# Performance work log

Measured on AMD Instinct MI355X. Metric: run time of the kernel, lower is better.

The kernel has to match this reference:

```python
import jax, jax.numpy as jnp
import numpy as np

B, T, D, H, Dh = 2, 2048, 2048, 16, 128


def setup_inputs() -> dict:
    key = jax.random.key(0)
    ks = jax.random.split(key, 9)
    s = 0.02
    return {
        "x": jax.random.normal(ks[0], (B, T, D), jnp.float32),
        "Wq": jax.random.normal(ks[1], (H, D, Dh), jnp.float32) * s,
        "bq": jax.random.normal(ks[2], (H, Dh), jnp.float32) * s,
        "Wk": jax.random.normal(ks[3], (H, D, Dh), jnp.float32) * s,
        "bk": jax.random.normal(ks[4], (H, Dh), jnp.float32) * s,
        "Wv": jax.random.normal(ks[5], (H, D, Dh), jnp.float32) * s,
        "bv": jax.random.normal(ks[6], (H, Dh), jnp.float32) * s,
        "Wp": jax.random.normal(ks[7], (D, D), jnp.float32) * s,
        "bp": jax.random.normal(ks[8], (D,), jnp.float32) * s,
    }


def reference(x, Wq, bq, Wk, bk, Wv, bv, Wp, bp):
    # per-head projections (stacked): [B, H, T, Dh]
    q = jnp.einsum("btd,hde->bhte", x, Wq) + bq[None, :, None, :]
    k = jnp.einsum("btd,hde->bhte", x, Wk) + bk[None, :, None, :]
    v = jnp.einsum("btd,hde->bhte", x, Wv) + bv[None, :, None, :]
    scale = Dh ** -0.5
    att = jnp.einsum("bhte,bhse->bhts", q, k) * scale  # [B,H,T,T]
    causal = jnp.tril(jnp.ones((T, T), bool))
    att = jnp.where(causal, att, -jnp.inf)
    att = jax.nn.softmax(att, axis=-1)
    # dropout p=0.0 -> identity
    out = jnp.einsum("bhts,bhse->bhte", att, v)  # [B,H,T,Dh]
    out = out.transpose(0, 2, 1, 3).reshape(B, T, H * Dh)  # concat heads
    return out @ Wp.T if False else jnp.einsum("btd,ed->bte", out, Wp.T) if False else out @ Wp + bp
```

## Files before the change

### kernel.cpp

```cpp
#include <hip/hip_runtime.h>
#include <hip/hip_bf16.h>
#include <math.h>

typedef __attribute__((ext_vector_type(8))) short bf16x8;
typedef __attribute__((ext_vector_type(4))) float f32x4;
typedef __attribute__((ext_vector_type(16))) float f32x16;

__device__ __forceinline__ unsigned short f2b(float f) {
    union { float f; unsigned u; } a; a.f = f;
    unsigned r = a.u + 0x7FFFu + ((a.u >> 16) & 1u);
    return (unsigned short)(r >> 16);
}

__device__ __forceinline__ void gl_lds16(const unsigned short* g, unsigned short* l) {
    __builtin_amdgcn_global_load_lds(
        (const __attribute__((address_space(1))) unsigned int*)g,
        (__attribute__((address_space(3))) unsigned int*)l,
        16, 0, 0);
}

#define SCALE2 0.12751744716529944f

__global__ __launch_bounds__(256) void prep_kernel(
    const float* __restrict__ x,
    const float* __restrict__ Wq, const float* __restrict__ Wk,
    const float* __restrict__ Wv, const float* __restrict__ Wp,
    unsigned short* __restrict__ xb, unsigned short* __restrict__ wt,
    unsigned short* __restrict__ wpt) {
    __shared__ float tile_s[32][33];
    int bid = blockIdx.x;
    int tx = threadIdx.x, ty = threadIdx.y;
    if (bid < 12288) {
        int z = bid >> 8;
        int tile = bid & 255;
        int c0 = (tile & 3) * 32, r0 = (tile >> 2) * 32;
        int mat = z >> 4, hh = z & 15;
        const float* src = ((mat == 0) ? Wq : (mat == 1) ? Wk : Wv) + (size_t)hh * 2048 * 128;
        unsigned short* dst = wt + (size_t)z * 128 * 2048;
#pragma unroll
        for (int i = 0; i < 32; i += 8)
            tile_s[ty + i][tx] = src[(size_t)(r0 + ty + i) * 128 + c0 + tx];
        __syncthreads();
#pragma unroll
        for (int i = 0; i < 32; i += 8)
            dst[(size_t)(c0 + ty + i) * 2048 + r0 + tx] = f2b(tile_s[tx][ty + i]);
    } else if (bid < 16384) {
        int tile = bid - 12288;
        int c0 = (tile & 63) * 32, r0 = (tile >> 6) * 32;
#pragma unroll
        for (int i = 0; i < 32; i += 8)
            tile_s[ty + i][tx] = Wp[(size_t)(r0 + ty + i) * 2048 + c0 + tx];
        __syncthreads();
#pragma unroll
        for (int i = 0; i < 32; i += 8)
            wpt[(size_t)(c0 + ty + i) * 2048 + r0 + tx] = f2b(tile_s[tx][ty + i]);
    } else {
        int base = (bid - 16384) * 1024 + ty * 32 + tx;
#pragma unroll
        for (int rep = 0; rep < 4; ++rep) {
            int i = base + rep * 256;
            float4 v = ((const float4*)x)[i];
            ushort4 o;
            o.x = f2b(v.x); o.y = f2b(v.y); o.z = f2b(v.z); o.w = f2b(v.w);
            ((ushort4*)xb)[i] = o;
        }
    }
}

constexpr int BKg = 64;

__global__ __launch_bounds__(256) void qkv_gemm_kernel(
    const unsigned short* __restrict__ xb,
    const unsigned short* __restrict__ wt,
    const float* __restrict__ bq, const float* __restrict__ bkb, const float* __restrict__ bvb,
    unsigned short* __restrict__ q, unsigned short* __restrict__ k, unsigned short* __restrict__ vt) {
    __shared__ unsigned short sA[128 * 64];
    __shared__ unsigned short sB[128 * 64];
    int cb = blockIdx.x;
    int m0 = blockIdx.y * 128;
    int tid = threadIdx.x;
    int lane = tid & 63, w = tid >> 6;
    int wm = w >> 1, wn = w & 1;
    int l32 = lane & 31, kh = lane >> 5;
    int srow = lane >> 3;
    int gcol = ((lane & 7) ^ srow) * 8;
    int swz = l32 & 7;

    f32x16 acc[2][2] = {};
    const unsigned short* aBase = xb + (size_t)m0 * 2048;
    const unsigned short* bBase = wt + (size_t)cb * 128 * 2048;

    for (int k0 = 0; k0 < 2048; k0 += BKg) {
#pragma unroll
        for (int p = 0; p < 4; ++p) {
            int row = w * 32 + p * 8 + srow;
            gl_lds16(aBase + (size_t)row * 2048 + k0 + gcol, sA + (w * 32 + p * 8) * 64);
            gl_lds16(bBase + (size_t)row * 2048 + k0 + gcol, sB + (w * 32 + p * 8) * 64);
        }
        __syncthreads();
#pragma unroll
        for (int kst = 0; kst < 4; ++kst) {
            int chunk = kst * 2 + kh;
            bf16x8 af[2], bfr[2];
#pragma unroll
            for (int a = 0; a < 2; ++a)
                af[a] = *(const bf16x8*)(sA + (wm * 64 + a * 32 + l32) * 64 + (chunk ^ swz) * 8);
#pragma unroll
            for (int b = 0; b < 2; ++b)
                bfr[b] = *(const bf16x8*)(sB + (wn * 64 + b * 32 + l32) * 64 + (chunk ^ swz) * 8);
#pragma unroll
            for (int a = 0; a < 2; ++a)
#pragma unroll
                for (int b = 0; b < 2; ++b)
                    acc[a][b] = __builtin_amdgcn_mfma_f32_32x32x16_bf16(af[a], bfr[b], acc[a][b], 0, 0, 0);
        }
        __syncthreads();
    }

    int mat = cb >> 4, h = cb & 15;
    const float* bias = (mat == 0) ? bq : (mat == 1) ? bkb : bvb;
    unsigned short* outqk = (mat == 0) ? q : k;
    float postscale = (mat == 0) ? SCALE2 : 1.0f;
#pragma unroll
    for (int a = 0; a < 2; ++a) {
#pragma unroll
        for (int b = 0; b < 2; ++b) {
            int col = wn * 64 + b * 32 + l32;
            float bb = bias[h * 128 + col];
            if (mat < 2) {
#pragma unroll
                for (int reg = 0; reg < 16; ++reg) {
                    int gr = m0 + wm * 64 + a * 32 + (reg & 3) + 8 * (reg >> 2) + 4 * kh;
                    int bi = gr >> 11, t = gr & 2047;
                    outqk[((size_t)(bi * 16 + h) * 2048 + t) * 128 + col] =
                        f2b((acc[a][b][reg] + bb) * postscale);
                }
            } else {
#pragma unroll
                for (int rg = 0; rg < 4; ++rg) {
                    int gr = m0 + wm * 64 + a * 32 + 8 * rg + 4 * kh;
                    int bi = gr >> 11, t = gr & 2047;
                    ushort4 pk;
                    pk.x = f2b(acc[a][b][rg * 4 + 0] + bb);
                    pk.y = f2b(acc[a][b][rg * 4 + 1] + bb);
                    pk.z = f2b(acc[a][b][rg * 4 + 2] + bb);
                    pk.w = f2b(acc[a][b][rg * 4 + 3] + bb);
                    *(ushort4*)(vt + ((size_t)(bi * 16 + h) * 128 + col) * 2048 + t) = pk;
                }
            }
        }
    }
}

__global__ __launch_bounds__(256) void attn_kernel(
    const unsigned short* __restrict__ qg,
    const unsigned short* __restrict__ kg,
    const unsigned short* __restrict__ vg,
    unsigned short* __restrict__ og) {
    constexpr int LDP = 72;
    __shared__ unsigned short sK[2][64 * 128];
    __shared__ unsigned short sV[2][128 * 64];
    __shared__ unsigned short sP[4 * 16 * LDP];

    int bh = blockIdx.x;
    int t0 = (31 - (int)blockIdx.y) * 64;
    int tid = threadIdx.x;
    int lane = tid & 63, w = tid >> 6;
    int ln = lane & 15, quad = lane >> 4;
    int swz = ln & 7;

    const unsigned short* qb = qg + (size_t)bh * 2048 * 128;
    const unsigned short* kb = kg + (size_t)bh * 2048 * 128;
    const unsigned short* vb = vg + (size_t)bh * 128 * 2048;

    bf16x8 qf[4];
#pragma unroll
    for (int c = 0; c < 4; ++c)
        qf[c] = *(const bf16x8*)(qb + (size_t)(t0 + w * 16 + ln) * 128 + c * 32 + quad * 8);

    f32x4 oacc[8] = {};
    float lst[4] = {0.f, 0.f, 0.f, 0.f};

    int nblk = t0 / 64 + 1;

    int kr = lane >> 4, km = lane & 15;
    int vr = lane >> 3, vm = lane & 7;

    {
        int s0 = 0;
#pragma unroll
        for (int p = 0; p < 4; ++p) {
            int krow = w * 16 + p * 4;
            int rswk = (krow + kr) & 7;
            int kch = (km & 8) | ((km & 7) ^ rswk);
            gl_lds16(kb + (size_t)(s0 + krow + kr) * 128 + kch * 8, sK[0] + krow * 128);
            int vrow = w * 32 + p * 8;
            int vch = vm ^ vr;
            gl_lds16(vb + (size_t)(vrow + vr) * 2048 + s0 + vch * 8, sV[0] + vrow * 64);
        }
    }

    for (int jb = 0; jb < nblk; ++jb) {
        int s0 = jb * 64;
        int buf = jb & 1;
        __syncthreads();
        if (jb + 1 < nblk) {
            int s1 = s0 + 64;
#pragma unroll
            for (int p = 0; p < 4; ++p) {
                int krow = w * 16 + p * 4;
                int rswk = (krow + kr) & 7;
                int kch = (km & 8) | ((km & 7) ^ rswk);
                gl_lds16(kb + (size_t)(s1 + krow + kr) * 128 + kch * 8, sK[buf ^ 1] + krow * 128);
                int vrow = w * 32 + p * 8;
                int vch = vm ^ vr;
                gl_lds16(vb + (size_t)(vrow + vr) * 2048 + s1 + vch * 8, sV[buf ^ 1] + vrow * 64);
            }
        }
        bool diag = (jb == nblk - 1);

        f32x4 sacc[4] = {};
#pragma unroll
        for (int c = 0; c < 4; ++c) {
            bf16x8 bfr[4];
#pragma unroll
            for (int j = 0; j < 4; ++j) {
                int ch = c * 4 + quad;
                int pos = (ch & 8) | ((ch ^ swz) & 7);
                bfr[j] = *(const bf16x8*)(sK[buf] + (j * 16 + ln) * 128 + pos * 8);
            }
#pragma unroll
            for (int j = 0; j < 4; ++j)
                sacc[j] = __builtin_amdgcn_mfma_f32_16x16x32_bf16(qf[c], bfr[j], sacc[j], 0, 0, 0);
        }
#pragma unroll
        for (int r = 0; r < 4; ++r) {
            int t = t0 + w * 16 + quad * 4 + r;
            float p_[4];
#pragma unroll
            for (int j = 0; j < 4; ++j) {
                float e_ = exp2f(sacc[j][r]);
                if (diag && (s0 + j * 16 + ln > t)) e_ = 0.f;
                p_[j] = e_;
                sP[(w * 16 + quad * 4 + r) * LDP + j * 16 + ln] = f2b(e_);
            }
            lst[r] += (p_[0] + p_[1]) + (p_[2] + p_[3]);
        }
#pragma unroll
        for (int c2 = 0; c2 < 2; ++c2) {
            bf16x8 af, bfr[8];
            af = *(const bf16x8*)(sP + (w * 16 + ln) * LDP + c2 * 32 + quad * 8);
#pragma unroll
            for (int jj = 0; jj < 8; ++jj) {
                int pos = (c2 * 4 + quad) ^ swz;
                bfr[jj] = *(const bf16x8*)(sV[buf] + (jj * 16 + ln) * 64 + pos * 8);
            }
#pragma unroll
            for (int jj = 0; jj < 8; ++jj)
                oacc[jj] = __builtin_amdgcn_mfma_f32_16x16x32_bf16(af, bfr[jj], oacc[jj], 0, 0, 0);
        }
    }

#pragma unroll
    for (int r = 0; r < 4; ++r) {
        int t = t0 + w * 16 + quad * 4 + r;
        float lsum = lst[r];
#pragma unroll
        for (int m_ = 8; m_ >= 1; m_ >>= 1)
            lsum += __shfl_xor(lsum, m_, 64);
        float inv = 1.f / lsum;
#pragma unroll
        for (int jj = 0; jj < 8; ++jj) {
            int e = jj * 16 + ln;
            og[((size_t)bh * 2048 + t) * 128 + e] = f2b(oacc[jj][r] * inv);
        }
    }
}

__global__ __launch_bounds__(256) void proj_gemm_kernel(
    const unsigned short* __restrict__ og,
    const unsigned short* __restrict__ wpt,
    const float* __restrict__ bp,
    float* __restrict__ out) {
    __shared__ unsigned short sA[128 * 64];
    __shared__ unsigned short sB[128 * 64];
    int cb = blockIdx.x;
    int m0 = blockIdx.y * 128;
    int b_ = m0 >> 11, t0_ = m0 & 2047;
    int tid = threadIdx.x;
    int lane = tid & 63, w = tid >> 6;
    int wm = w >> 1, wn = w & 1;
    int l32 = lane & 31, kh = lane >> 5;
    int srow = lane >> 3;
    int gcol = ((lane & 7) ^ srow) * 8;
    int swz = l32 & 7;

    f32x16 acc[2][2] = {};
    const unsigned short* bBase = wpt + (size_t)cb * 128 * 2048;

    for (int k0 = 0; k0 < 2048; k0 += BKg) {
        int h = k0 >> 7, e0 = k0 & 127;
        const unsigned short* aBase = og + ((size_t)(b_ * 16 + h) * 2048 + t0_) * 128 + e0;
#pragma unroll
        for (int p = 0; p < 4; ++p) {
            int row = w * 32 + p * 8 + srow;
            gl_lds16(aBase + (size_t)row * 128 + gcol, sA + (w * 32 + p * 8) * 64);
            gl_lds16(bBase + (size_t)row * 2048 + k0 + gcol, sB + (w * 32 + p * 8) * 64);
        }
        __syncthreads();
#pragma unroll
        for (int kst = 0; kst < 4; ++kst) {
            int chunk = kst * 2 + kh;
            bf16x8 af[2], bfr[2];
#pragma unroll
            for (int a = 0; a < 2; ++a)
                af[a] = *(const bf16x8*)(sA + (wm * 64 + a * 32 + l32) * 64 + (chunk ^ swz) * 8);
#pragma unroll
            for (int b = 0; b < 2; ++b)
                bfr[b] = *(const bf16x8*)(sB + (wn * 64 + b * 32 + l32) * 64 + (chunk ^ swz) * 8);
#pragma unroll
            for (int a = 0; a < 2; ++a)
#pragma unroll
                for (int b = 0; b < 2; ++b)
                    acc[a][b] = __builtin_amdgcn_mfma_f32_32x32x16_bf16(af[a], bfr[b], acc[a][b], 0, 0, 0);
        }
        __syncthreads();
    }

#pragma unroll
    for (int a = 0; a < 2; ++a)
#pragma unroll
        for (int b = 0; b < 2; ++b) {
            int col = cb * 128 + wn * 64 + b * 32 + l32;
            float bias = bp[col];
#pragma unroll
            for (int reg = 0; reg < 16; ++reg) {
                int row = m0 + wm * 64 + a * 32 + (reg & 3) + 8 * (reg >> 2) + 4 * kh;
                out[(size_t)row * 2048 + col] = acc[a][b][reg] + bias;
            }
        }
}

extern "C" void kernel_launch(void* const* d_in, const int* in_sizes, int n_in,
                              void* d_out, int out_size, void* d_ws, size_t ws_size,
                              hipStream_t stream) {
    const float* x  = (const float*)d_in[0];
    const float* Wq = (const float*)d_in[1];
    const float* bq = (const float*)d_in[2];
    const float* Wk = (const float*)d_in[3];
    const float* bk = (const float*)d_in[4];
    const float* Wv = (const float*)d_in[5];
    const float* bv = (const float*)d_in[6];
    const float* Wp = (const float*)d_in[7];
    const float* bp = (const float*)d_in[8];
    float* out = (float*)d_out;

    char* ws = (char*)d_ws;
    unsigned short* xb  = (unsigned short*)(ws);
    unsigned short* wt  = (unsigned short*)(ws + 16777216);
    unsigned short* wpt = (unsigned short*)(ws + 41943040);
    unsigned short* q   = (unsigned short*)(ws + 50331648);
    unsigned short* k   = (unsigned short*)(ws + 67108864);
    unsigned short* vt  = (unsigned short*)(ws + 83886080);
    unsigned short* o   = (unsigned short*)(ws + 100663296);

    dim3 tb(32, 8);
    prep_kernel<<<18432, tb, 0, stream>>>(x, Wq, Wk, Wv, Wp, xb, wt, wpt);
    qkv_gemm_kernel<<<dim3(48, 32), 256, 0, stream>>>(xb, wt, bq, bk, bv, q, k, vt);
    attn_kernel<<<dim3(32, 32), 256, 0, stream>>>(q, k, vt, o);
    proj_gemm_kernel<<<dim3(16, 32), 256, 0, stream>>>(o, wpt, bp, out);
}
```

Measured before the change: 363.7 us.

## Rewrite QKV GEMM with 256x256 tiles, double-buffered LDS pipeline, 512 threads

The QKV projection GEMM moves from 128x128 tiles on 256 threads to 256x256 tiles on 512 threads (8 waves). Global-to-LDS loads for the next k-tiles are double-buffered and interleaved with MFMA phases, using explicit vmcnt waits, barriers, and setprio around the MFMA bursts. This targets global load latency and operand reuse, at the cost of 128KB of LDS per block, fewer blocks (384), and a fragile hand-written wait schedule.

```diff
diff --git a/kernel.cpp b/kernel.cpp
--- a/kernel.cpp
+++ b/kernel.cpp
@@ -69,83 +69,121 @@
 
 constexpr int BKg = 64;
 
-__global__ __launch_bounds__(256) void qkv_gemm_kernel(
+__global__ __launch_bounds__(512, 2) void qkv_gemm_kernel(
     const unsigned short* __restrict__ xb,
     const unsigned short* __restrict__ wt,
     const float* __restrict__ bq, const float* __restrict__ bkb, const float* __restrict__ bvb,
     unsigned short* __restrict__ q, unsigned short* __restrict__ k, unsigned short* __restrict__ vt) {
-    __shared__ unsigned short sA[128 * 64];
-    __shared__ unsigned short sB[128 * 64];
-    int cb = blockIdx.x;
-    int m0 = blockIdx.y * 128;
+    __shared__ unsigned short sA[2][256 * 64];
+    __shared__ unsigned short sB[2][256 * 64];
+    int nb = blockIdx.x;
+    int m0 = blockIdx.y * 256;
     int tid = threadIdx.x;
     int lane = tid & 63, w = tid >> 6;
-    int wm = w >> 1, wn = w & 1;
+    int wm = w >> 2, wn = w & 3;
     int l32 = lane & 31, kh = lane >> 5;
-    int srow = lane >> 3;
-    int gcol = ((lane & 7) ^ srow) * 8;
     int swz = l32 & 7;
-
-    f32x16 acc[2][2] = {};
-    const unsigned short* aBase = xb + (size_t)m0 * 2048;
-    const unsigned short* bBase = wt + (size_t)cb * 128 * 2048;
-
-    for (int k0 = 0; k0 < 2048; k0 += BKg) {
-#pragma unroll
-        for (int p = 0; p < 4; ++p) {
-            int row = w * 32 + p * 8 + srow;
-            gl_lds16(aBase + (size_t)row * 2048 + k0 + gcol, sA + (w * 32 + p * 8) * 64);
-            gl_lds16(bBase + (size_t)row * 2048 + k0 + gcol, sB + (w * 32 + p * 8) * 64);
-        }
-        __syncthreads();
-#pragma unroll
-        for (int kst = 0; kst < 4; ++kst) {
-            int chunk = kst * 2 + kh;
-            bf16x8 af[2], bfr[2];
-#pragma unroll
-            for (int a = 0; a < 2; ++a)
-                af[a] = *(const bf16x8*)(sA + (wm * 64 + a * 32 + l32) * 64 + (chunk ^ swz) * 8);
-#pragma unroll
-            for (int b = 0; b < 2; ++b)
-                bfr[b] = *(const bf16x8*)(sB + (wn * 64 + b * 32 + l32) * 64 + (chunk ^ swz) * 8);
-#pragma unroll
-            for (int a = 0; a < 2; ++a)
-#pragma unroll
-                for (int b = 0; b < 2; ++b)
-                    acc[a][b] = __builtin_amdgcn_mfma_f32_32x32x16_bf16(af[a], bfr[b], acc[a][b], 0, 0, 0);
-        }
-        __syncthreads();
-    }
-
-    int mat = cb >> 4, h = cb & 15;
+    int lr = lane >> 3, lc = lane & 7;
+    int gco = (lc ^ lr) << 3;
+
+    const unsigned short* aB = xb + (size_t)m0 * 2048;
+    const unsigned short* bB = wt + (size_t)nb * 256 * 2048;
+
+    auto stgA = [&](int bf_, int kt, int qq) {
+        int ar = (w >> 2) * 128 + qq * 32 + (w & 3) * 8;
+        gl_lds16(aB + (size_t)(ar + lr) * 2048 + kt * 64 + gco, &sA[bf_][ar * 64]);
+    };
+    auto stgB = [&](int bf_, int kt, int hh) {
+        int br = hh * 64 + w * 8;
+        gl_lds16(bB + (size_t)(br + lr) * 2048 + kt * 64 + gco, &sB[bf_][br * 64]);
+    };
+
+    f32x16 acc[4][2] = {};
+
+#pragma unroll
+    for (int u = 0; u < 4; ++u) { stgA(0, 0, u); stgB(0, 0, u); }
+#pragma unroll
+    for (int u = 0; u < 3; ++u) { stgA(1, 1, u); stgB(1, 1, u); }
+    asm volatile("s_waitcnt vmcnt(6)");
+    __builtin_amdgcn_s_barrier();
+
+    for (int t = 0; t < 32; ++t) {
+        int bf_ = t & 1;
+        bf16x8 bfr[2][4], af[4];
+        if (t + 1 < 32) { stgA(bf_ ^ 1, t + 1, 3); stgB(bf_ ^ 1, t + 1, 3); }
+#pragma unroll
+        for (int ni = 0; ni < 2; ++ni)
+#pragma unroll
+            for (int kst = 0; kst < 4; ++kst)
+                bfr[ni][kst] = *(const bf16x8*)&sB[bf_][(wn * 64 + ni * 32 + l32) * 64 + (((kst * 2 + kh) ^ swz) << 3)];
+#pragma unroll
+        for (int kst = 0; kst < 4; ++kst)
+            af[kst] = *(const bf16x8*)&sA[bf_][(wm * 128 + l32) * 64 + (((kst * 2 + kh) ^ swz) << 3)];
+        __builtin_amdgcn_s_barrier();
+        asm volatile("s_waitcnt lgkmcnt(0)");
+        __builtin_amdgcn_sched_barrier(0);
+        __builtin_amdgcn_s_setprio(1);
+#pragma unroll
+        for (int kst = 0; kst < 4; ++kst)
+#pragma unroll
+            for (int ni = 0; ni < 2; ++ni)
+                acc[0][ni] = __builtin_amdgcn_mfma_f32_32x32x16_bf16(af[kst], bfr[ni][kst], acc[0][ni], 0, 0, 0);
+        __builtin_amdgcn_s_setprio(0);
+        __builtin_amdgcn_s_barrier();
+#pragma unroll
+        for (int qq = 1; qq < 4; ++qq) {
+            if (t + 2 < 32) { stgA(bf_, t + 2, qq - 1); stgB(bf_, t + 2, qq - 1); }
+#pragma unroll
+            for (int kst = 0; kst < 4; ++kst)
+                af[kst] = *(const bf16x8*)&sA[bf_][(wm * 128 + qq * 32 + l32) * 64 + (((kst * 2 + kh) ^ swz) << 3)];
+            if (qq == 3) {
+                if (t < 30) asm volatile("s_waitcnt vmcnt(6)");
+                else        asm volatile("s_waitcnt vmcnt(0)");
+            }
+            __builtin_amdgcn_s_barrier();
+            asm volatile("s_waitcnt lgkmcnt(0)");
+            __builtin_amdgcn_sched_barrier(0);
+            __builtin_amdgcn_s_setprio(1);
+#pragma unroll
+            for (int kst = 0; kst < 4; ++kst)
+#pragma unroll
+                for (int ni = 0; ni < 2; ++ni)
+                    acc[qq][ni] = __builtin_amdgcn_mfma_f32_32x32x16_bf16(af[kst], bfr[ni][kst], acc[qq][ni], 0, 0, 0);
+            __builtin_amdgcn_s_setprio(0);
+            __builtin_amdgcn_s_barrier();
+        }
+    }
+
+    int mat = nb >> 3;
+    int h = (nb * 2 + (wn >> 1)) & 15;
     const float* bias = (mat == 0) ? bq : (mat == 1) ? bkb : bvb;
     unsigned short* outqk = (mat == 0) ? q : k;
     float postscale = (mat == 0) ? SCALE2 : 1.0f;
 #pragma unroll
-    for (int a = 0; a < 2; ++a) {
-#pragma unroll
-        for (int b = 0; b < 2; ++b) {
-            int col = wn * 64 + b * 32 + l32;
-            float bb = bias[h * 128 + col];
+    for (int mi = 0; mi < 4; ++mi) {
+#pragma unroll
+        for (int ni = 0; ni < 2; ++ni) {
+            int ch = (wn & 1) * 64 + ni * 32 + l32;
+            float bb = bias[h * 128 + ch];
             if (mat < 2) {
 #pragma unroll
                 for (int reg = 0; reg < 16; ++reg) {
-                    int gr = m0 + wm * 64 + a * 32 + (reg & 3) + 8 * (reg >> 2) + 4 * kh;
-                    int bi = gr >> 11, t = gr & 2047;
-                    outqk[((size_t)(bi * 16 + h) * 2048 + t) * 128 + col] =
-                        f2b((acc[a][b][reg] + bb) * postscale);
+                    int gr = m0 + wm * 128 + mi * 32 + (reg & 3) + 8 * (reg >> 2) + 4 * kh;
+                    int bi = gr >> 11, tt = gr & 2047;
+                    outqk[((size_t)(bi * 16 + h) * 2048 + tt) * 128 + ch] =
+                        f2b((acc[mi][ni][reg] + bb) * postscale);
                 }
             } else {
 #pragma unroll
                 for (int rg = 0; rg < 4; ++rg) {
-                    int gr = m0 + wm * 64 + a * 32 + 8 * rg + 4 * kh;
-                    int bi = gr >> 11, t = gr & 2047;
+                    int gr = m0 + wm * 128 + mi * 32 + 8 * rg + 4 * kh;
+                    int bi = gr >> 11, tt = gr & 2047;
                     ushort4 pk;
-                    pk.x = f2b(acc[a][b][rg * 4 + 0] + bb);
-                    pk.y = f2b(acc[a][b][rg * 4 + 1] + bb);
-                    pk.z = f2b(acc[a][b][rg * 4 + 2] + bb);
-                    pk.w = f2b(acc[a][b][rg * 4 + 3] + bb);
-                    *(ushort4*)(vt + ((size_t)(bi * 16 + h) * 128 + col) * 2048 + t) = pk;
+                    pk.x = f2b(acc[mi][ni][rg * 4 + 0] + bb);
+                    pk.y = f2b(acc[mi][ni][rg * 4 + 1] + bb);
+                    pk.z = f2b(acc[mi][ni][rg * 4 + 2] + bb);
+                    pk.w = f2b(acc[mi][ni][rg * 4 + 3] + bb);
+                    *(ushort4*)(vt + ((size_t)(bi * 16 + h) * 128 + ch) * 2048 + tt) = pk;
                 }
             }
         }
@@ -366,7 +404,7 @@
 
     dim3 tb(32, 8);
     prep_kernel<<<18432, tb, 0, stream>>>(x, Wq, Wk, Wv, Wp, xb, wt, wpt);
-    qkv_gemm_kernel<<<dim3(48, 32), 256, 0, stream>>>(xb, wt, bq, bk, bv, q, k, vt);
+    qkv_gemm_kernel<<<dim3(24, 16), 512, 0, stream>>>(xb, wt, bq, bk, bv, q, k, vt);
     attn_kernel<<<dim3(32, 32), 256, 0, stream>>>(q, k, vt, o);
     proj_gemm_kernel<<<dim3(16, 32), 256, 0, stream>>>(o, wpt, bp, out);
 }
```

Result: slower. 449.1 us (+23.5%).

## Enlarge attention query tile to 128 rows with 8 waves sharing K/V tiles

Applied to the files above, without the earlier changes.

The attention kernel now processes 128 query rows per block with 512 threads (8 waves) instead of 64 rows with 4 waves. Each K/V tile staged into shared memory is reused by twice as many waves, which halves global K/V traffic and cuts per-block loads per thread. Waves whose rows lie entirely before a key block skip its compute, and the diagonal mask test is done per wave. The P scratch buffer changes from padded rows to an XOR-swizzled layout, trading the padding for index arithmetic. Risks are idle waves on diagonal blocks, fewer blocks for load balance, and higher register and LDS pressure per block.

```diff
diff --git a/kernel.cpp b/kernel.cpp
--- a/kernel.cpp
+++ b/kernel.cpp
@@ -152,51 +152,52 @@
     }
 }
 
-__global__ __launch_bounds__(256) void attn_kernel(
+__global__ __launch_bounds__(512) void attn_kernel(
     const unsigned short* __restrict__ qg,
     const unsigned short* __restrict__ kg,
     const unsigned short* __restrict__ vg,
     unsigned short* __restrict__ og) {
-    constexpr int LDP = 72;
     __shared__ unsigned short sK[2][64 * 128];
     __shared__ unsigned short sV[2][128 * 64];
-    __shared__ unsigned short sP[4 * 16 * LDP];
+    __shared__ unsigned short sP[128 * 64];
 
     int bh = blockIdx.x;
-    int t0 = (31 - (int)blockIdx.y) * 64;
+    int qb = 15 - (int)blockIdx.y;
+    int t0 = qb * 128;
     int tid = threadIdx.x;
     int lane = tid & 63, w = tid >> 6;
     int ln = lane & 15, quad = lane >> 4;
     int swz = ln & 7;
 
-    const unsigned short* qb = qg + (size_t)bh * 2048 * 128;
+    const unsigned short* qp = qg + (size_t)bh * 2048 * 128;
     const unsigned short* kb = kg + (size_t)bh * 2048 * 128;
     const unsigned short* vb = vg + (size_t)bh * 128 * 2048;
 
     bf16x8 qf[4];
 #pragma unroll
     for (int c = 0; c < 4; ++c)
-        qf[c] = *(const bf16x8*)(qb + (size_t)(t0 + w * 16 + ln) * 128 + c * 32 + quad * 8);
+        qf[c] = *(const bf16x8*)(qp + (size_t)(t0 + w * 16 + ln) * 128 + c * 32 + quad * 8);
 
     f32x4 oacc[8] = {};
     float lst[4] = {0.f, 0.f, 0.f, 0.f};
 
-    int nblk = t0 / 64 + 1;
+    int nblk = 2 * qb + 2;
+    int rowlo = t0 + w * 16;
+    int rowhi = rowlo + 15;
 
     int kr = lane >> 4, km = lane & 15;
     int vr = lane >> 3, vm = lane & 7;
 
     {
-        int s0 = 0;
-#pragma unroll
-        for (int p = 0; p < 4; ++p) {
-            int krow = w * 16 + p * 4;
+#pragma unroll
+        for (int p = 0; p < 2; ++p) {
+            int krow = w * 8 + p * 4;
             int rswk = (krow + kr) & 7;
             int kch = (km & 8) | ((km & 7) ^ rswk);
-            gl_lds16(kb + (size_t)(s0 + krow + kr) * 128 + kch * 8, sK[0] + krow * 128);
-            int vrow = w * 32 + p * 8;
+            gl_lds16(kb + (size_t)(krow + kr) * 128 + kch * 8, sK[0] + krow * 128);
+            int vrow = w * 16 + p * 8;
             int vch = vm ^ vr;
-            gl_lds16(vb + (size_t)(vrow + vr) * 2048 + s0 + vch * 8, sV[0] + vrow * 64);
+            gl_lds16(vb + (size_t)(vrow + vr) * 2048 + vch * 8, sV[0] + vrow * 64);
         }
     }
 
@@ -207,17 +208,18 @@
         if (jb + 1 < nblk) {
             int s1 = s0 + 64;
 #pragma unroll
-            for (int p = 0; p < 4; ++p) {
-                int krow = w * 16 + p * 4;
+            for (int p = 0; p < 2; ++p) {
+                int krow = w * 8 + p * 4;
                 int rswk = (krow + kr) & 7;
                 int kch = (km & 8) | ((km & 7) ^ rswk);
                 gl_lds16(kb + (size_t)(s1 + krow + kr) * 128 + kch * 8, sK[buf ^ 1] + krow * 128);
-                int vrow = w * 32 + p * 8;
+                int vrow = w * 16 + p * 8;
                 int vch = vm ^ vr;
                 gl_lds16(vb + (size_t)(vrow + vr) * 2048 + s1 + vch * 8, sV[buf ^ 1] + vrow * 64);
             }
         }
-        bool diag = (jb == nblk - 1);
+        if (s0 > rowhi) continue;
+        bool diag = (s0 + 63 > rowlo);
 
         f32x4 sacc[4] = {};
 #pragma unroll
@@ -235,21 +237,24 @@
         }
 #pragma unroll
         for (int r = 0; r < 4; ++r) {
-            int t = t0 + w * 16 + quad * 4 + r;
+            int rr = w * 16 + quad * 4 + r;
+            int t = t0 + rr;
+            int rs = rr & 7;
             float p_[4];
 #pragma unroll
             for (int j = 0; j < 4; ++j) {
                 float e_ = exp2f(sacc[j][r]);
                 if (diag && (s0 + j * 16 + ln > t)) e_ = 0.f;
                 p_[j] = e_;
-                sP[(w * 16 + quad * 4 + r) * LDP + j * 16 + ln] = f2b(e_);
+                int col = j * 16 + ln;
+                sP[rr * 64 + (((col >> 3) ^ rs) << 3) + (col & 7)] = f2b(e_);
             }
             lst[r] += (p_[0] + p_[1]) + (p_[2] + p_[3]);
         }
 #pragma unroll
         for (int c2 = 0; c2 < 2; ++c2) {
             bf16x8 af, bfr[8];
-            af = *(const bf16x8*)(sP + (w * 16 + ln) * LDP + c2 * 32 + quad * 8);
+            af = *(const bf16x8*)(sP + (w * 16 + ln) * 64 + (((c2 * 4 + quad) ^ swz) << 3));
 #pragma unroll
             for (int jj = 0; jj < 8; ++jj) {
                 int pos = (c2 * 4 + quad) ^ swz;
@@ -367,6 +372,6 @@
     dim3 tb(32, 8);
     prep_kernel<<<18432, tb, 0, stream>>>(x, Wq, Wk, Wv, Wp, xb, wt, wpt);
     qkv_gemm_kernel<<<dim3(48, 32), 256, 0, stream>>>(xb, wt, bq, bk, bv, q, k, vt);
-    attn_kernel<<<dim3(32, 32), 256, 0, stream>>>(q, k, vt, o);
+    attn_kernel<<<dim3(32, 16), 512, 0, stream>>>(q, k, vt, o);
     proj_gemm_kernel<<<dim3(16, 32), 256, 0, stream>>>(o, wpt, bp, out);
 }
```

Measured after the change: 377.4 us. 3.8% more time.

## Switch attention kernel to 32x32x16 MFMA with split-KV warp pairs and LDS merge

Applied to the files above, without the earlier changes.

The attention kernel moves from 16x16x32 to 32x32x16 bf16 MFMA tiles. Each wave pair shares a 32-row query tile, and each wave handles half of the 64-key block, so partial outputs and row sums are merged through LDS at the end. This aims to raise MFMA efficiency and cut LDS fragment reads per FLOP. In exchange it adds a final cross-wave reduction and uses more accumulator registers, which can lower occupancy. The score is split across two accumulators (s0a + s1a) over alternating K chunks.

```diff
diff --git a/kernel.cpp b/kernel.cpp
--- a/kernel.cpp
+++ b/kernel.cpp
@@ -157,47 +157,44 @@
     const unsigned short* __restrict__ kg,
     const unsigned short* __restrict__ vg,
     unsigned short* __restrict__ og) {
-    constexpr int LDP = 72;
     __shared__ unsigned short sK[2][64 * 128];
     __shared__ unsigned short sV[2][128 * 64];
-    __shared__ unsigned short sP[4 * 16 * LDP];
+    __shared__ unsigned short sP[4][32 * 36];
 
     int bh = blockIdx.x;
     int t0 = (31 - (int)blockIdx.y) * 64;
     int tid = threadIdx.x;
     int lane = tid & 63, w = tid >> 6;
-    int ln = lane & 15, quad = lane >> 4;
-    int swz = ln & 7;
-
-    const unsigned short* qb = qg + (size_t)bh * 2048 * 128;
+    int l32 = lane & 31, kh = lane >> 5;
+    int rg = w >> 1;
+    int kvh = w & 1;
+    int sw = l32 & 7;
+
+    const unsigned short* qp = qg + (size_t)bh * 2048 * 128;
     const unsigned short* kb = kg + (size_t)bh * 2048 * 128;
     const unsigned short* vb = vg + (size_t)bh * 128 * 2048;
 
-    bf16x8 qf[4];
-#pragma unroll
-    for (int c = 0; c < 4; ++c)
-        qf[c] = *(const bf16x8*)(qb + (size_t)(t0 + w * 16 + ln) * 128 + c * 32 + quad * 8);
-
-    f32x4 oacc[8] = {};
-    float lst[4] = {0.f, 0.f, 0.f, 0.f};
+    bf16x8 qf[8];
+#pragma unroll
+    for (int c = 0; c < 8; ++c)
+        qf[c] = *(const bf16x8*)(qp + (size_t)(t0 + rg * 32 + l32) * 128 + c * 16 + kh * 8);
+
+    f32x16 oaccv[4] = {};
+    float lst[16] = {};
 
     int nblk = t0 / 64 + 1;
 
     int kr = lane >> 4, km = lane & 15;
     int vr = lane >> 3, vm = lane & 7;
 
-    {
-        int s0 = 0;
-#pragma unroll
-        for (int p = 0; p < 4; ++p) {
-            int krow = w * 16 + p * 4;
-            int rswk = (krow + kr) & 7;
-            int kch = (km & 8) | ((km & 7) ^ rswk);
-            gl_lds16(kb + (size_t)(s0 + krow + kr) * 128 + kch * 8, sK[0] + krow * 128);
-            int vrow = w * 32 + p * 8;
-            int vch = vm ^ vr;
-            gl_lds16(vb + (size_t)(vrow + vr) * 2048 + s0 + vch * 8, sV[0] + vrow * 64);
-        }
+#pragma unroll
+    for (int p = 0; p < 4; ++p) {
+        int krow = w * 16 + p * 4;
+        int rswk = (krow + kr) & 7;
+        int kch = (km & 8) | ((km & 7) ^ rswk);
+        gl_lds16(kb + (size_t)(krow + kr) * 128 + kch * 8, sK[0] + krow * 128);
+        int vrow = w * 32 + p * 8;
+        gl_lds16(vb + (size_t)(vrow + vr) * 2048 + (vm ^ vr) * 8, sV[0] + vrow * 64);
     }
 
     for (int jb = 0; jb < nblk; ++jb) {
@@ -213,66 +210,78 @@
                 int kch = (km & 8) | ((km & 7) ^ rswk);
                 gl_lds16(kb + (size_t)(s1 + krow + kr) * 128 + kch * 8, sK[buf ^ 1] + krow * 128);
                 int vrow = w * 32 + p * 8;
-                int vch = vm ^ vr;
-                gl_lds16(vb + (size_t)(vrow + vr) * 2048 + s1 + vch * 8, sV[buf ^ 1] + vrow * 64);
+                gl_lds16(vb + (size_t)(vrow + vr) * 2048 + s1 + (vm ^ vr) * 8, sV[buf ^ 1] + vrow * 64);
             }
         }
         bool diag = (jb == nblk - 1);
 
-        f32x4 sacc[4] = {};
+        f32x16 s0a = {}, s1a = {};
 #pragma unroll
         for (int c = 0; c < 4; ++c) {
-            bf16x8 bfr[4];
-#pragma unroll
-            for (int j = 0; j < 4; ++j) {
-                int ch = c * 4 + quad;
-                int pos = (ch & 8) | ((ch ^ swz) & 7);
-                bfr[j] = *(const bf16x8*)(sK[buf] + (j * 16 + ln) * 128 + pos * 8);
-            }
-#pragma unroll
-            for (int j = 0; j < 4; ++j)
-                sacc[j] = __builtin_amdgcn_mfma_f32_16x16x32_bf16(qf[c], bfr[j], sacc[j], 0, 0, 0);
-        }
-#pragma unroll
-        for (int r = 0; r < 4; ++r) {
-            int t = t0 + w * 16 + quad * 4 + r;
-            float p_[4];
-#pragma unroll
-            for (int j = 0; j < 4; ++j) {
-                float e_ = exp2f(sacc[j][r]);
-                if (diag && (s0 + j * 16 + ln > t)) e_ = 0.f;
-                p_[j] = e_;
-                sP[(w * 16 + quad * 4 + r) * LDP + j * 16 + ln] = f2b(e_);
-            }
-            lst[r] += (p_[0] + p_[1]) + (p_[2] + p_[3]);
-        }
-#pragma unroll
-        for (int c2 = 0; c2 < 2; ++c2) {
-            bf16x8 af, bfr[8];
-            af = *(const bf16x8*)(sP + (w * 16 + ln) * LDP + c2 * 32 + quad * 8);
-#pragma unroll
-            for (int jj = 0; jj < 8; ++jj) {
-                int pos = (c2 * 4 + quad) ^ swz;
-                bfr[jj] = *(const bf16x8*)(sV[buf] + (jj * 16 + ln) * 64 + pos * 8);
-            }
-#pragma unroll
-            for (int jj = 0; jj < 8; ++jj)
-                oacc[jj] = __builtin_amdgcn_mfma_f32_16x16x32_bf16(af, bfr[jj], oacc[jj], 0, 0, 0);
-        }
-    }
-
-#pragma unroll
-    for (int r = 0; r < 4; ++r) {
-        int t = t0 + w * 16 + quad * 4 + r;
-        float lsum = lst[r];
-#pragma unroll
-        for (int m_ = 8; m_ >= 1; m_ >>= 1)
-            lsum += __shfl_xor(lsum, m_, 64);
-        float inv = 1.f / lsum;
-#pragma unroll
-        for (int jj = 0; jj < 8; ++jj) {
-            int e = jj * 16 + ln;
-            og[((size_t)bh * 2048 + t) * 128 + e] = f2b(oacc[jj][r] * inv);
+            int ch0 = (2 * c) * 2 + kh, ch1 = (2 * c + 1) * 2 + kh;
+            int p0 = (ch0 & 8) | ((ch0 ^ sw) & 7);
+            int p1 = (ch1 & 8) | ((ch1 ^ sw) & 7);
+            bf16x8 k0 = *(const bf16x8*)(sK[buf] + (kvh * 32 + l32) * 128 + p0 * 8);
+            bf16x8 k1 = *(const bf16x8*)(sK[buf] + (kvh * 32 + l32) * 128 + p1 * 8);
+            s0a = __builtin_amdgcn_mfma_f32_32x32x16_bf16(qf[2 * c], k0, s0a, 0, 0, 0);
+            s1a = __builtin_amdgcn_mfma_f32_32x32x16_bf16(qf[2 * c + 1], k1, s1a, 0, 0, 0);
+        }
+
+        int kvc = s0 + kvh * 32 + l32;
+#pragma unroll
+        for (int r = 0; r < 16; ++r) {
+            int roff = (r & 3) + 8 * (r >> 2) + 4 * kh;
+            float e_ = exp2f(s0a[r] + s1a[r]);
+            if (diag && (kvc > t0 + rg * 32 + roff)) e_ = 0.f;
+            lst[r] += e_;
+            sP[w][roff * 36 + l32] = f2b(e_);
+        }
+
+#pragma unroll
+        for (int kst = 0; kst < 2; ++kst) {
+            bf16x8 pf = *(const bf16x8*)(sP[w] + l32 * 36 + kst * 16 + kh * 8);
+#pragma unroll
+            for (int nb = 0; nb < 4; ++nb) {
+                int ch = kvh * 4 + kst * 2 + kh;
+                bf16x8 vf = *(const bf16x8*)(sV[buf] + (nb * 32 + l32) * 64 + (ch ^ sw) * 8);
+                oaccv[nb] = __builtin_amdgcn_mfma_f32_32x32x16_bf16(pf, vf, oaccv[nb], 0, 0, 0);
+            }
+        }
+    }
+
+#pragma unroll
+    for (int r = 0; r < 16; ++r) {
+#pragma unroll
+        for (int m_ = 16; m_ >= 1; m_ >>= 1)
+            lst[r] += __shfl_xor(lst[r], m_, 64);
+    }
+
+    __syncthreads();
+    float* oS = (float*)sK;
+    float* lS = (float*)sV;
+    if (kvh) {
+#pragma unroll
+        for (int nb = 0; nb < 4; ++nb)
+#pragma unroll
+            for (int r = 0; r < 16; ++r)
+                oS[rg * 4096 + (nb * 16 + r) * 64 + lane] = oaccv[nb][r];
+        if (l32 == 0)
+#pragma unroll
+            for (int r = 0; r < 16; ++r)
+                lS[rg * 32 + (r & 3) + 8 * (r >> 2) + 4 * kh] = lst[r];
+    }
+    __syncthreads();
+    if (!kvh) {
+#pragma unroll
+        for (int r = 0; r < 16; ++r) {
+            int roff = (r & 3) + 8 * (r >> 2) + 4 * kh;
+            float inv = 1.f / (lst[r] + lS[rg * 32 + roff]);
+            int row = t0 + rg * 32 + roff;
+#pragma unroll
+            for (int nb = 0; nb < 4; ++nb) {
+                float ov = oaccv[nb][r] + oS[rg * 4096 + (nb * 16 + r) * 64 + lane];
+                og[((size_t)bh * 2048 + row) * 128 + nb * 32 + l32] = f2b(ov * inv);
+            }
         }
     }
 }
```

Measured after the change: 387.3 us. 6.5% more time.
